# Kernel optimization log

Measured on AMD Instinct MI355X. Metric: run time of the kernel, lower is better.

## Reference

```python
import jax, jax.numpy as jnp
import numpy as np

B, S, D = 4, 2048, 768
H = 12
DH = D // H  # 64
DF = 2048
THETA = 10000.0
EPS = 1e-5


def setup_inputs() -> dict:
    key = jax.random.key(0)
    ks = jax.random.split(key, 8)
    sc = 0.02  # keep activations numerically tame
    return {
        "x": jax.random.normal(ks[0], (B, S, D), jnp.float32),
        "ln1_w": jnp.ones((D,), jnp.float32),
        "ln2_w": jnp.ones((D,), jnp.float32),
        "p_q": jax.random.normal(ks[1], (D, D), jnp.float32) * sc,
        "p_k": jax.random.normal(ks[2], (D, D), jnp.float32) * sc,
        "p_v": jax.random.normal(ks[3], (D, D), jnp.float32) * sc,
        "p_o": jax.random.normal(ks[4], (D, D), jnp.float32) * sc,
        "w1": jax.random.normal(ks[5], (DF, D), jnp.float32) * sc,
        "w2": jax.random.normal(ks[6], (D, DF), jnp.float32) * sc,
        "w3": jax.random.normal(ks[7], (DF, D), jnp.float32) * sc,
    }


def _rmsnorm(x, w):
    # matches torch: fp32 compute, mean-square + eps
    rms = jnp.sqrt(jnp.mean(x * x, axis=-1, keepdims=True) + EPS)
    return x / rms * w


def _rope(t):
    # t: [B, H, S, DH]; rotation per RoPE matrix: pairs (2k, 2k+1)
    pos = jnp.arange(S, dtype=jnp.float32)[:, None]            # [S,1]
    k = jnp.arange(DH // 2, dtype=jnp.float32)[None, :]        # [1,DH/2]
    ang = pos / (THETA ** (2.0 * k / DH))                      # [S,DH/2]
    cos, sin = jnp.cos(ang), jnp.sin(ang)
    t2 = t.reshape(*t.shape[:-1], DH // 2, 2)
    x0, x1 = t2[..., 0], t2[..., 1]
    o0 = cos * x0 - sin * x1
    o1 = sin * x0 + cos * x1
    return jnp.stack([o0, o1], axis=-1).reshape(t.shape)


def reference(x, ln1_w, ln2_w, p_q, p_k, p_v, p_o, w1, w2, w3):
    # --- attention sublayer ---
    h = _rmsnorm(x, ln1_w)                                     # [B,S,D]
    Wq = p_q.reshape(H, DH, D)
    Wk = p_k.reshape(H, DH, D)
    Wv = p_v.reshape(H, DH, D)
    q = _rope(jnp.einsum('bsd,hed->bhse', h, Wq))              # [B,H,S,DH]
    k = _rope(jnp.einsum('bsd,hed->bhse', h, Wk))
    v = jnp.einsum('bsd,hed->bhse', h, Wv)
    scores = jnp.einsum('bhqe,bhke->bhqk', q, k)               # [B,H,S,S]
    mask = jnp.tril(jnp.ones((S, S), bool))
    scores = jnp.where(mask, scores, -jnp.inf)
    attn = jax.nn.softmax(scores / jnp.sqrt(jnp.float32(DH)), axis=-1)
    ctx = jnp.einsum('bhqk,bhke->bhqe', attn, v)               # [B,H,S,DH]
    ctx = jnp.transpose(ctx, (0, 2, 1, 3)).reshape(B, S, D)    # [B,S,D]
    x = x + ctx @ p_o.T
    # --- SwiGLU FFN sublayer ---
    h2 = _rmsnorm(x, ln2_w)
    u1 = h2 @ w1.T
    u1 = u1 * jax.nn.sigmoid(u1)                               # SiLU
    u3 = h2 @ w3.T
    x = x + (u1 * u3) @ w2.T
    return x
```

## Files before the change

kernel.cpp:

```cpp
#include <hip/hip_runtime.h>
#include <stdint.h>

#define B_  4
#define S_  2048
#define D_  768
#define H_  12
#define DH_ 64
#define DF_ 2048
#define M_  (B_*S_)
#define NQKV 2304
#define N13  4096

typedef __attribute__((ext_vector_type(8))) short bf16x8;
typedef __attribute__((ext_vector_type(4))) short bf16x4;
typedef __attribute__((ext_vector_type(4))) float f32x4;
typedef unsigned short u16;

#if !defined(__HIP_DEVICE_COMPILE__)
  #define MFMA_K16(A,B,C) (C)
#elif __has_builtin(__builtin_amdgcn_mfma_f32_16x16x16_bf16)
  #define MFMA_K16(A,B,C) __builtin_amdgcn_mfma_f32_16x16x16_bf16((A),(B),(C),0,0,0)
#else
  #define MFMA_K16(A,B,C) __builtin_amdgcn_mfma_f32_16x16x16bf16_1k((A),(B),(C),0,0,0)
#endif

__device__ __forceinline__ float bf2f(u16 v) {
  union { uint32_t u; float f; } x; x.u = ((uint32_t)v) << 16; return x.f;
}
__device__ __forceinline__ u16 f2bf(float f) {
  union { float f; uint32_t u; } x; x.f = f;
  uint32_t r = x.u + 0x7FFFu + ((x.u >> 16) & 1u);
  return (u16)(r >> 16);
}
__device__ __forceinline__ void gl_lds16(const u16* g, u16* l) {
  __builtin_amdgcn_global_load_lds((const __attribute__((address_space(1))) uint32_t*)g,
                                   (__attribute__((address_space(3))) uint32_t*)l, 16, 0, 0);
}

__global__ __launch_bounds__(256) void cast_all_kernel(const float* __restrict__ pq,
                                                       const float* __restrict__ pk,
                                                       const float* __restrict__ pv,
                                                       const float* __restrict__ po,
                                                       const float* __restrict__ w2,
                                                       u16* __restrict__ wqkv,
                                                       u16* __restrict__ wob,
                                                       u16* __restrict__ w2b) {
  int bidx = blockIdx.x;
  const float* src; u16* dst; int off;
  if (bidx < 576)       { src = pq; dst = wqkv;           off = bidx; }
  else if (bidx < 1152) { src = pk; dst = wqkv + 589824;  off = bidx - 576; }
  else if (bidx < 1728) { src = pv; dst = wqkv + 1179648; off = bidx - 1152; }
  else if (bidx < 2304) { src = po; dst = wob;            off = bidx - 1728; }
  else                  { src = w2; dst = w2b;            off = bidx - 2304; }
  int i = off * 256 + threadIdx.x;
  float4 v = ((const float4*)src)[i];
  ushort4 o;
  o.x = f2bf(v.x); o.y = f2bf(v.y); o.z = f2bf(v.z); o.w = f2bf(v.w);
  ((ushort4*)dst)[i] = o;
}

__global__ __launch_bounds__(192) void cast_w13_kernel(const float* __restrict__ w1,
                                                       const float* __restrict__ w3,
                                                       u16* __restrict__ out) {
  int j = blockIdx.x, which = blockIdx.y;
  const float* src = (which ? w3 : w1) + (size_t)j * D_;
  int fr = (j >> 4) * 32 + (j & 15) + which * 16;
  u16* dst = out + (size_t)fr * D_;
  int t = threadIdx.x;
  float4 v = ((const float4*)src)[t];
  ushort4 o;
  o.x = f2bf(v.x); o.y = f2bf(v.y); o.z = f2bf(v.z); o.w = f2bf(v.w);
  ((ushort4*)dst)[t] = o;
}

__global__ __launch_bounds__(256) void rmsnorm_kernel(const float* __restrict__ x,
                                                      const float* __restrict__ w,
                                                      u16* __restrict__ out) {
  int row = blockIdx.x, tid = threadIdx.x;
  const float* xr = x + (size_t)row * D_;
  float v0 = xr[tid], v1 = xr[tid + 256], v2 = xr[tid + 512];
  float ss = v0 * v0 + v1 * v1 + v2 * v2;
  #pragma unroll
  for (int m = 32; m >= 1; m >>= 1) ss += __shfl_xor(ss, m, 64);
  __shared__ float red[4];
  if ((tid & 63) == 0) red[tid >> 6] = ss;
  __syncthreads();
  float tot = red[0] + red[1] + red[2] + red[3];
  float r = rsqrtf(tot * (1.0f / D_) + 1e-5f);
  u16* o = out + (size_t)row * D_;
  o[tid]       = f2bf(v0 * r * w[tid]);
  o[tid + 256] = f2bf(v1 * r * w[tid + 256]);
  o[tid + 512] = f2bf(v2 * r * w[tid + 512]);
}

template<int MT, int EPI>
__global__ __launch_bounds__(256) void gemm_bt_kernel(const u16* __restrict__ A,
                                                      const u16* __restrict__ W,
                                                      void* __restrict__ Cout,
                                                      const float* __restrict__ res,
                                                      u16* __restrict__ vTout,
                                                      int K, int N) {
  constexpr int ABELEMS = MT * 64 + 128 * 64;
  constexpr int SMELEMS = (EPI == 3 && 128 * 132 > ABELEMS) ? 128 * 132 : ABELEMS;
  __shared__ __align__(16) u16 smem[SMELEMS];
  u16* As = smem;
  u16* Bs = smem + MT * 64;
  constexpr int MI = MT / 32;
  int tid = threadIdx.x;
  int wave = tid >> 6, lane = tid & 63;
  int quad = lane >> 4, l16 = lane & 15;
  int wr = (wave >> 1) * (MT / 2), wc = (wave & 1) * 64;
  int m0 = blockIdx.y * MT, n0 = blockIdx.x * 128;
  f32x4 acc[MI][4] = {};
  for (int kt = 0; kt < K; kt += 64) {
    __syncthreads();
    #pragma unroll
    for (int i = 0; i < MT / 32; ++i) {
      int idx = i * 256 + tid;
      int r = idx >> 3, c = idx & 7;
      gl_lds16(&A[(size_t)(m0 + r) * K + kt + ((c ^ (r & 7)) * 8)], &As[(i * 256 + wave * 64) * 8]);
    }
    #pragma unroll
    for (int i = 0; i < 4; ++i) {
      int idx = i * 256 + tid;
      int r = idx >> 3, c = idx & 7;
      gl_lds16(&W[(size_t)(n0 + r) * K + kt + ((c ^ (r & 7)) * 8)], &Bs[(i * 256 + wave * 64) * 8]);
    }
    __syncthreads();
    #pragma unroll
    for (int ks = 0; ks < 2; ++ks) {
      bf16x8 af[MI], bf[4];
      int sw = ((ks * 4 + quad) ^ (l16 & 7)) * 8;
      #pragma unroll
      for (int t = 0; t < MI; ++t)
        af[t] = *(const bf16x8*)&As[(wr + t * 16 + l16) * 64 + sw];
      #pragma unroll
      for (int t = 0; t < 4; ++t)
        bf[t] = *(const bf16x8*)&Bs[(wc + t * 16 + l16) * 64 + sw];
      #pragma unroll
      for (int mt = 0; mt < MI; ++mt)
        #pragma unroll
        for (int nt = 0; nt < 4; ++nt)
          acc[mt][nt] = __builtin_amdgcn_mfma_f32_16x16x32_bf16(af[mt], bf[nt], acc[mt][nt], 0, 0, 0);
    }
  }

  if (EPI == 3 && n0 >= 1536) {
    __syncthreads();
    #pragma unroll
    for (int mt = 0; mt < MI; ++mt) {
      int sloc = wr + mt * 16 + quad * 4;
      #pragma unroll
      for (int nt = 0; nt < 4; ++nt) {
        int col = wc + nt * 16 + l16;
        ushort4 o;
        o.x = f2bf(acc[mt][nt][0]); o.y = f2bf(acc[mt][nt][1]);
        o.z = f2bf(acc[mt][nt][2]); o.w = f2bf(acc[mt][nt][3]);
        *(ushort4*)&smem[col * 132 + sloc] = o;
      }
    }
    __syncthreads();
    int b = m0 >> 11, sblk = m0 & 2047;
    #pragma unroll
    for (int i = 0; i < 8; ++i) {
      int idx = i * 256 + tid;
      int row = idx >> 4, c16 = idx & 15;
      uint4 d = *(const uint4*)&smem[row * 132 + c16 * 8];
      int vg = n0 - 1536 + row;
      int h = vg >> 6, dh = vg & 63;
      *(uint4*)&vTout[((size_t)(b * H_ + h) * 64 + dh) * (size_t)S_ + sblk + c16 * 8] = d;
    }
  } else if (EPI == 3) {
    bool isq = (n0 < 768);
    float osc = isq ? 0.18033688f : 1.0f;
    #pragma unroll
    for (int mt = 0; mt < MI; ++mt) {
      int r0 = m0 + wr + mt * 16 + quad * 4;
      int pos0 = r0 & 2047;
      #pragma unroll
      for (int nt = 0; nt < 4; ++nt) {
        int col = n0 + wc + nt * 16 + l16;
        int kk = (col & 63) >> 1;
        float freq = exp2f(-0.41524101186092035f * (float)kk);
        bool odd = (col & 1);
        #pragma unroll
        for (int r = 0; r < 4; ++r) {
          float own = acc[mt][nt][r];
          float pv = __shfl_xor(own, 1, 64);
          float ang = (float)(pos0 + r) * freq;
          float sv, cv;
          __sincosf(ang, &sv, &cv);
          float o = odd ? (sv * pv + cv * own) : (cv * own - sv * pv);
          ((u16*)Cout)[(size_t)(r0 + r) * N + col] = f2bf(o * osc);
        }
      }
    }
  } else {
    #pragma unroll
    for (int mt = 0; mt < MI; ++mt) {
      #pragma unroll
      for (int r = 0; r < 4; ++r) {
        int gr = m0 + wr + mt * 16 + quad * 4 + r;
        if (EPI == 2) {
          #pragma unroll
          for (int np = 0; np < 2; ++np) {
            float u1v = acc[mt][np * 2][r], u3v = acc[mt][np * 2 + 1][r];
            float sg = 1.0f / (1.0f + __builtin_amdgcn_exp2f(-u1v * 1.44269504f));
            float g = u1v * sg * u3v;
            int gc = (n0 >> 1) + (wave & 1) * 32 + np * 16 + l16;
            ((u16*)Cout)[(size_t)gr * (N >> 1) + gc] = f2bf(g);
          }
        } else {
          #pragma unroll
          for (int nt = 0; nt < 4; ++nt) {
            int gc = n0 + wc + nt * 16 + l16;
            size_t off = (size_t)gr * N + gc;
            float vv = acc[mt][nt][r];
            if (EPI == 1) ((float*)Cout)[off] = vv + res[off];
            else          ((u16*)Cout)[off] = f2bf(vv);
          }
        }
      }
    }
  }
}

__global__ __launch_bounds__(256, 4) void attn_kernel(const u16* __restrict__ qkv,
                                                      const u16* __restrict__ vT,
                                                      u16* __restrict__ ctx) {
  __shared__ __align__(16) u16 Ks[128 * 64];
  __shared__ __align__(16) u16 Vt[64 * 128];
  int bh = blockIdx.x;
  int qt = 15 - blockIdx.y;
  int b = bh / H_, h = bh % H_;
  const u16* qbase = qkv + (size_t)b * S_ * NQKV + h * DH_;
  const u16* kbase = qbase + 768;
  const u16* vtb   = vT + (size_t)bh * 64 * S_;
  int tid = threadIdx.x, wave = tid >> 6, lane = tid & 63;
  int quad = lane >> 4, l16 = lane & 15;
  const float MFIX = 12.0f;

  bf16x8 qf[2][2];
  #pragma unroll
  for (int mt = 0; mt < 2; ++mt) {
    int qrow = qt * 128 + wave * 32 + mt * 16 + l16;
    qf[mt][0] = *(const bf16x8*)&qbase[(size_t)qrow * NQKV + quad * 8];
    qf[mt][1] = *(const bf16x8*)&qbase[(size_t)qrow * NQKV + 32 + quad * 8];
  }
  f32x4 oacc[2][4] = {};
  float lsum[2] = {0.f, 0.f};
  int nkt = qt + 1;
  for (int kt = 0; kt < nkt; ++kt) {
    __syncthreads();
    #pragma unroll
    for (int i = 0; i < 4; ++i) {
      int idx = i * 256 + tid;
      int r = idx >> 3, c = idx & 7;
      gl_lds16(&kbase[(size_t)(kt * 128 + r) * NQKV + ((c ^ (r & 7)) * 8)],
               &Ks[(i * 256 + wave * 64) * 8]);
    }
    #pragma unroll
    for (int i = 0; i < 4; ++i) {
      int idx = i * 256 + tid;
      int d = idx >> 4, c16 = idx & 15;
      gl_lds16(&vtb[(size_t)d * S_ + kt * 128 + ((c16 ^ (d & 15)) * 8)],
               &Vt[(i * 256 + wave * 64) * 8]);
    }
    __syncthreads();
    bool diag = (kt == nkt - 1);
    #pragma unroll
    for (int t = 0; t < 8; ++t) {
      if (diag && t > 2 * wave + 1) break;
      f32x4 sc0 = {}, sc1 = {};
      #pragma unroll
      for (int c = 0; c < 2; ++c) {
        bf16x8 kf = *(const bf16x8*)&Ks[(t * 16 + l16) * 64 + (((c * 4 + quad) ^ (l16 & 7)) * 8)];
        sc0 = __builtin_amdgcn_mfma_f32_16x16x32_bf16(kf, qf[0][c], sc0, 0, 0, 0);
        sc1 = __builtin_amdgcn_mfma_f32_16x16x32_bf16(kf, qf[1][c], sc1, 0, 0, 0);
      }
      bf16x4 pf[2];
      #pragma unroll
      for (int mt = 0; mt < 2; ++mt) {
        f32x4 sv = mt ? sc1 : sc0;
        float p[4];
        #pragma unroll
        for (int r = 0; r < 4; ++r) p[r] = __builtin_amdgcn_exp2f(sv[r] - MFIX);
        if (diag) {
          int ql = wave * 32 + mt * 16 + l16;
          #pragma unroll
          for (int r = 0; r < 4; ++r)
            if (t * 16 + quad * 4 + r > ql) p[r] = 0.f;
        }
        lsum[mt] += (p[0] + p[1]) + (p[2] + p[3]);
        uint32_t lo = ((__float_as_uint(p[0]) + 0x8000u) >> 16) |
                      ((__float_as_uint(p[1]) + 0x8000u) & 0xFFFF0000u);
        uint32_t hi = ((__float_as_uint(p[2]) + 0x8000u) >> 16) |
                      ((__float_as_uint(p[3]) + 0x8000u) & 0xFFFF0000u);
        uint2 pk; pk.x = lo; pk.y = hi;
        pf[mt] = *(bf16x4*)&pk;
      }
      #pragma unroll
      for (int n = 0; n < 4; ++n) {
        bf16x4 vf = *(const bf16x4*)&Vt[(n * 16 + l16) * 128 +
                                        (((t * 2 + (quad >> 1)) ^ l16) * 8) + (quad & 1) * 4];
        oacc[0][n] = MFMA_K16(vf, pf[0], oacc[0][n]);
        oacc[1][n] = MFMA_K16(vf, pf[1], oacc[1][n]);
      }
    }
  }
  #pragma unroll
  for (int mt = 0; mt < 2; ++mt) {
    float l = lsum[mt];
    l += __shfl_xor(l, 16, 64);
    l += __shfl_xor(l, 32, 64);
    float inv = 1.0f / l;
    int qrow = qt * 128 + wave * 32 + mt * 16 + l16;
    #pragma unroll
    for (int n = 0; n < 4; ++n) {
      ushort4 o;
      o.x = f2bf(oacc[mt][n][0] * inv);
      o.y = f2bf(oacc[mt][n][1] * inv);
      o.z = f2bf(oacc[mt][n][2] * inv);
      o.w = f2bf(oacc[mt][n][3] * inv);
      *(ushort4*)&ctx[(size_t)(b * S_ + qrow) * D_ + h * DH_ + n * 16 + quad * 4] = o;
    }
  }
}

#define WQKV_OFF 0u
#define W13_OFF  3538944u
#define W2_OFF   9830400u
#define WO_OFF   12976128u
#define HB_OFF   14155776u
#define QKV_OFF  26738688u
#define VT_OFF   64487424u
#define X1_OFF   77070336u
#define G_OFF    102236160u

extern "C" void kernel_launch(void* const* d_in, const int* in_sizes, int n_in,
                              void* d_out, int out_size, void* d_ws, size_t ws_size,
                              hipStream_t stream) {
  const float* x    = (const float*)d_in[0];
  const float* ln1w = (const float*)d_in[1];
  const float* ln2w = (const float*)d_in[2];
  const float* pq   = (const float*)d_in[3];
  const float* pk   = (const float*)d_in[4];
  const float* pv   = (const float*)d_in[5];
  const float* po   = (const float*)d_in[6];
  const float* w1   = (const float*)d_in[7];
  const float* w2   = (const float*)d_in[8];
  const float* w3   = (const float*)d_in[9];
  char* ws = (char*)d_ws;
  u16* wqkv = (u16*)(ws + WQKV_OFF);
  u16* w13b = (u16*)(ws + W13_OFF);
  u16* w2b  = (u16*)(ws + W2_OFF);
  u16* wob  = (u16*)(ws + WO_OFF);
  u16* hb   = (u16*)(ws + HB_OFF);
  u16* qkvb = (u16*)(ws + QKV_OFF);
  u16* vtb  = (u16*)(ws + VT_OFF);
  u16* cb   = (u16*)(ws + HB_OFF);
  float* x1 = (float*)(ws + X1_OFF);
  u16* h2b  = (u16*)(ws + VT_OFF);
  u16* gb   = (u16*)(ws + G_OFF);

  cast_all_kernel<<<3840, 256, 0, stream>>>(pq, pk, pv, po, w2, wqkv, wob, w2b);
  cast_w13_kernel<<<dim3(2048, 2), 192, 0, stream>>>(w1, w3, w13b);

  rmsnorm_kernel<<<M_, 256, 0, stream>>>(x, ln1w, hb);
  gemm_bt_kernel<128, 3><<<dim3(18, 64), 256, 0, stream>>>(hb, wqkv, qkvb, nullptr, vtb, 768, NQKV);
  attn_kernel<<<dim3(48, 16), 256, 0, stream>>>(qkvb, vtb, cb);
  gemm_bt_kernel<64, 1><<<dim3(6, 128), 256, 0, stream>>>(cb, wob, x1, x, nullptr, 768, 768);

  rmsnorm_kernel<<<M_, 256, 0, stream>>>(x1, ln2w, h2b);
  gemm_bt_kernel<128, 2><<<dim3(32, 64), 256, 0, stream>>>(h2b, w13b, gb, nullptr, nullptr, 768, N13);
  gemm_bt_kernel<64, 1><<<dim3(6, 128), 256, 0, stream>>>(gb, w2b, (float*)d_out, x1, nullptr, 2048, 768);
}
```

Baseline: 356.3 us.

## Use 256x256-tile 8-wave pipelined GEMM for the fused W1/W3 SwiGLU projection

Adds a new GEMM kernel with 256x256 block tiles, 512 threads and double-buffered LDS staged through global-to-LDS loads. It splits each tile into quadrants so register fragment loads overlap MFMA issue, and raises wave priority around the MFMA blocks. It replaces the 128-tile kernel only for the W1/W3 projection with its SiLU-gating epilogue. This raises data reuse per block and hides load latency, at the cost of heavy barrier use, higher register and LDS pressure, and fewer blocks (512) to fill the GPU.

```diff
diff --git a/kernel.cpp b/kernel.cpp
--- a/kernel.cpp
+++ b/kernel.cpp
@@ -222,6 +222,207 @@
         }
       }
     }
+  }
+}
+
+#define FENCE() asm volatile("" ::: "memory")
+#define BAR() do { FENCE(); __builtin_amdgcn_s_barrier(); FENCE(); } while (0)
+#define LGKM0() do { asm volatile("s_waitcnt lgkmcnt(0)" ::: "memory"); \
+                     __builtin_amdgcn_sched_barrier(0); } while (0)
+
+template<int MH, int NH>
+__device__ __forceinline__ void quad_mfma(f32x4 (&acc)[2][4][2][2],
+                                          const bf16x8 (&ra)[4][2],
+                                          const bf16x8 (&rb)[2][2]) {
+  #pragma unroll
+  for (int ks = 0; ks < 2; ++ks)
+    #pragma unroll
+    for (int mt = 0; mt < 4; ++mt)
+      #pragma unroll
+      for (int nt = 0; nt < 2; ++nt)
+        acc[MH][mt][NH][nt] =
+          __builtin_amdgcn_mfma_f32_16x16x32_bf16(ra[mt][ks], rb[nt][ks], acc[MH][mt][NH][nt], 0, 0, 0);
+}
+
+__device__ __forceinline__ void ld_afrags(bf16x8 (&rr)[4][2], const u16* base,
+                                          int wrow, int l16, int quad) {
+  #pragma unroll
+  for (int mt = 0; mt < 4; ++mt)
+    #pragma unroll
+    for (int ks = 0; ks < 2; ++ks)
+      rr[mt][ks] = *(const bf16x8*)&base[(wrow + mt * 16 + l16) * 64 +
+                                         (((ks * 4 + quad) ^ (l16 & 7)) * 8)];
+}
+__device__ __forceinline__ void ld_bfrags(bf16x8 (&rr)[2][2], const u16* base,
+                                          int wrow, int l16, int quad) {
+  #pragma unroll
+  for (int nt = 0; nt < 2; ++nt)
+    #pragma unroll
+    for (int ks = 0; ks < 2; ++ks)
+      rr[nt][ks] = *(const bf16x8*)&base[(wrow + nt * 16 + l16) * 64 +
+                                         (((ks * 4 + quad) ^ (l16 & 7)) * 8)];
+}
+
+template<int EPI>
+__global__ __launch_bounds__(512, 2) void gemm256_kernel(const u16* __restrict__ A,
+                                                         const u16* __restrict__ W,
+                                                         void* __restrict__ Cout,
+                                                         const float* __restrict__ res,
+                                                         int K, int N) {
+  __shared__ __align__(16) u16 smem[2][2][2][128 * 64];
+  int tid = threadIdx.x;
+  int wave = tid >> 6, lane = tid & 63;
+  int quad = lane >> 4, l16 = lane & 15;
+  int wm = wave >> 2, wn = wave & 3;
+  int m0 = blockIdx.y * 256, n0 = blockIdx.x * 256;
+  const int T = K >> 6;
+  const int NI = T >> 1;
+
+  f32x4 acc[2][4][2][2] = {};
+  bf16x8 rAlo[4][2], rAhi[4][2], rBlo[2][2], rBhi[2][2];
+
+  int r0 = tid >> 3, c0 = tid & 7;
+  int sc0 = (c0 ^ (r0 & 7)) * 8;
+
+  #define STG(kt, ab, h) do {                                                        \
+    const u16* _s = (ab) ? W : A;                                                    \
+    int _b = ((ab) ? n0 : m0) + (h) * 128;                                           \
+    u16* _d = &smem[(kt) & 1][ab][h][wave * 512];                                    \
+    gl_lds16(&_s[(size_t)(_b + r0) * K + (kt) * 64 + sc0], _d);                      \
+    gl_lds16(&_s[(size_t)(_b + 64 + r0) * K + (kt) * 64 + sc0], _d + 4096);          \
+  } while (0)
+
+  int wrA = wm * 64, wrB = wn * 32;
+
+  STG(0, 0, 0); STG(0, 1, 0); STG(0, 1, 1); STG(0, 0, 1);
+  STG(1, 0, 0); STG(1, 1, 0); STG(1, 1, 1); STG(1, 0, 1);
+  asm volatile("s_waitcnt vmcnt(8)" ::: "memory");
+  BAR();
+  ld_afrags(rAlo, &smem[0][0][0][0], wrA, l16, quad);
+  ld_bfrags(rBlo, &smem[0][1][0][0], wrB, l16, quad);
+  BAR();
+
+  for (int i = 0; i < NI; ++i) {
+    int t2 = 2 * i + 2, t3 = 2 * i + 3;
+    bool more = (i + 1 < NI);
+    ld_bfrags(rBhi, &smem[0][1][1][0], wrB, l16, quad);
+    if (more) STG(t2, 0, 0);
+    BAR(); LGKM0();
+    __builtin_amdgcn_s_setprio(1);
+    quad_mfma<0, 0>(acc, rAlo, rBlo);
+    __builtin_amdgcn_s_setprio(0);
+    BAR();
+    ld_afrags(rAhi, &smem[0][0][1][0], wrA, l16, quad);
+    if (more) STG(t2, 1, 0);
+    BAR(); LGKM0();
+    __builtin_amdgcn_s_setprio(1);
+    quad_mfma<0, 1>(acc, rAlo, rBhi);
+    __builtin_amdgcn_s_setprio(0);
+    BAR();
+    if (more) STG(t2, 1, 1);
+    BAR(); LGKM0();
+    __builtin_amdgcn_s_setprio(1);
+    quad_mfma<1, 0>(acc, rAhi, rBlo);
+    __builtin_amdgcn_s_setprio(0);
+    if (more) asm volatile("s_waitcnt vmcnt(6)" ::: "memory");
+    else      asm volatile("s_waitcnt vmcnt(0)" ::: "memory");
+    BAR();
+    ld_afrags(rAlo, &smem[1][0][0][0], wrA, l16, quad);
+    ld_bfrags(rBlo, &smem[1][1][0][0], wrB, l16, quad);
+    if (more) STG(t2, 0, 1);
+    asm volatile("s_waitcnt lgkmcnt(8)" ::: "memory");
+    BAR(); LGKM0();
+    __builtin_amdgcn_s_setprio(1);
+    quad_mfma<1, 1>(acc, rAhi, rBhi);
+    __builtin_amdgcn_s_setprio(0);
+    BAR();
+    ld_bfrags(rBhi, &smem[1][1][1][0], wrB, l16, quad);
+    if (more) STG(t3, 0, 0);
+    BAR(); LGKM0();
+    __builtin_amdgcn_s_setprio(1);
+    quad_mfma<0, 0>(acc, rAlo, rBlo);
+    __builtin_amdgcn_s_setprio(0);
+    BAR();
+    ld_afrags(rAhi, &smem[1][0][1][0], wrA, l16, quad);
+    if (more) STG(t3, 1, 0);
+    BAR(); LGKM0();
+    __builtin_amdgcn_s_setprio(1);
+    quad_mfma<0, 1>(acc, rAlo, rBhi);
+    __builtin_amdgcn_s_setprio(0);
+    BAR();
+    if (more) STG(t3, 1, 1);
+    BAR(); LGKM0();
+    __builtin_amdgcn_s_setprio(1);
+    quad_mfma<1, 0>(acc, rAhi, rBlo);
+    __builtin_amdgcn_s_setprio(0);
+    if (more) asm volatile("s_waitcnt vmcnt(6)" ::: "memory");
+    else      asm volatile("s_waitcnt vmcnt(0)" ::: "memory");
+    BAR();
+    if (more) {
+      ld_afrags(rAlo, &smem[0][0][0][0], wrA, l16, quad);
+      ld_bfrags(rBlo, &smem[0][1][0][0], wrB, l16, quad);
+      STG(t3, 0, 1);
+    }
+    asm volatile("s_waitcnt lgkmcnt(8)" ::: "memory");
+    BAR(); LGKM0();
+    __builtin_amdgcn_s_setprio(1);
+    quad_mfma<1, 1>(acc, rAhi, rBhi);
+    __builtin_amdgcn_s_setprio(0);
+    BAR();
+  }
+  #undef STG
+
+  if (EPI == 2) {
+    const int Nh = N >> 1;
+    #pragma unroll
+    for (int mh = 0; mh < 2; ++mh)
+      #pragma unroll
+      for (int mt = 0; mt < 4; ++mt)
+        #pragma unroll
+        for (int r = 0; r < 4; ++r) {
+          int gr = m0 + mh * 128 + wm * 64 + mt * 16 + quad * 4 + r;
+          #pragma unroll
+          for (int nh = 0; nh < 2; ++nh) {
+            float u1v = acc[mh][mt][nh][0][r], u3v = acc[mh][mt][nh][1][r];
+            float sg = 1.0f / (1.0f + __builtin_amdgcn_exp2f(-u1v * 1.44269504f));
+            float g = u1v * sg * u3v;
+            int gc = (n0 >> 1) + nh * 64 + wn * 16 + l16;
+            ((u16*)Cout)[(size_t)gr * Nh + gc] = f2bf(g);
+          }
+        }
+  } else if (EPI == 1) {
+    #pragma unroll
+    for (int mh = 0; mh < 2; ++mh)
+      #pragma unroll
+      for (int mt = 0; mt < 4; ++mt)
+        #pragma unroll
+        for (int r = 0; r < 4; ++r) {
+          int gr = m0 + mh * 128 + wm * 64 + mt * 16 + quad * 4 + r;
+          #pragma unroll
+          for (int nh = 0; nh < 2; ++nh)
+            #pragma unroll
+            for (int nt = 0; nt < 2; ++nt) {
+              int gc = n0 + nh * 128 + wn * 32 + nt * 16 + l16;
+              size_t off = (size_t)gr * N + gc;
+              ((float*)Cout)[off] = acc[mh][mt][nh][nt][r] + res[off];
+            }
+        }
+  } else {
+    #pragma unroll
+    for (int mh = 0; mh < 2; ++mh)
+      #pragma unroll
+      for (int mt = 0; mt < 4; ++mt)
+        #pragma unroll
+        for (int r = 0; r < 4; ++r) {
+          int gr = m0 + mh * 128 + wm * 64 + mt * 16 + quad * 4 + r;
+          #pragma unroll
+          for (int nh = 0; nh < 2; ++nh)
+            #pragma unroll
+            for (int nt = 0; nt < 2; ++nt) {
+              int gc = n0 + nh * 128 + wn * 32 + nt * 16 + l16;
+              ((u16*)Cout)[(size_t)gr * N + gc] = f2bf(acc[mh][mt][nh][nt][r]);
+            }
+        }
   }
 }
 
@@ -372,6 +573,6 @@
   gemm_bt_kernel<64, 1><<<dim3(6, 128), 256, 0, stream>>>(cb, wob, x1, x, nullptr, 768, 768);
 
   rmsnorm_kernel<<<M_, 256, 0, stream>>>(x1, ln2w, h2b);
-  gemm_bt_kernel<128, 2><<<dim3(32, 64), 256, 0, stream>>>(h2b, w13b, gb, nullptr, nullptr, 768, N13);
+  gemm256_kernel<2><<<dim3(N13 / 256, M_ / 256), 512, 0, stream>>>(h2b, w13b, gb, nullptr, 768, N13);
   gemm_bt_kernel<64, 1><<<dim3(6, 128), 256, 0, stream>>>(gb, w2b, (float*)d_out, x1, nullptr, 2048, 768);
 }
```

After: 385.6 us. 8.2% more time.
